# Optimization experiments

Hardware: AMD Instinct MI355X
Metric: run time of the kernel (lower is better)

Reference implementation:

```python
import jax, jax.numpy as jnp
import numpy as np

DIM = 1024
HEADS = 16
DIM_HEAD = 64
INNER = HEADS * DIM_HEAD
ALPHA = 128.0
SCALE = DIM_HEAD ** -0.5 / ALPHA
EPS = 1e-5
MAX_NEG = -jnp.finfo(jnp.float32).max


def layernorm(x, g):
    # torch.var(unbiased=False) layernorm with learned gain, no bias
    mean = jnp.mean(x, axis=-1, keepdims=True)
    var = jnp.mean(jnp.square(x - mean), axis=-1, keepdims=True)
    return (x - mean) * jax.lax.rsqrt(var + EPS) * g


def setup_inputs() -> dict:
    key = jax.random.key(0)
    ks = jax.random.split(key, 8)
    b, n = 8, 1024
    x = jax.random.normal(ks[0], (b, n, DIM), dtype=jnp.float32)
    mask = jax.random.bernoulli(ks[1], 0.9, (b, n))  # bool padding mask
    g_in = jnp.ones((DIM,), jnp.float32)
    Wq = jax.random.normal(ks[2], (INNER, DIM), jnp.float32) * (DIM ** -0.5)
    Wkv = jax.random.normal(ks[3], (2 * DIM_HEAD, DIM), jnp.float32) * (DIM ** -0.5)
    null_kv = jax.random.normal(ks[4], (2, DIM_HEAD), jnp.float32)
    Wo = jax.random.normal(ks[5], (DIM, INNER), jnp.float32) * (INNER ** -0.5)
    g_out = jnp.ones((DIM,), jnp.float32)
    return {"x": x, "mask": mask, "g_in": g_in, "Wq": Wq, "Wkv": Wkv,
            "null_kv": null_kv, "Wo": Wo, "g_out": g_out}


def reference(x, mask, g_in, Wq, Wkv, null_kv, Wo, g_out):
    b, n, _ = x.shape
    context = x                      # context captured BEFORE norm
    xn = layernorm(x, g_in)
    q = (xn @ Wq.T).reshape(b, n, HEADS, DIM_HEAD).transpose(0, 2, 1, 3)  # b h n d
    q = q * SCALE
    kv = context @ Wkv.T             # b n 2d (single shared KV head: MQA)
    k, v = jnp.split(kv, 2, axis=-1)
    nk = jnp.broadcast_to(null_kv[0], (b, 1, DIM_HEAD))
    nv = jnp.broadcast_to(null_kv[1], (b, 1, DIM_HEAD))
    k = jnp.concatenate([nk, k], axis=1)   # b (n+1) d
    v = jnp.concatenate([nv, v], axis=1)
    sim = jnp.einsum('bhid,bjd->bhij', q, k)  # b h n (n+1)
    # padding mask, True prepended for null token
    m = jnp.pad(mask, ((0, 0), (1, 0)), constant_values=True)
    sim = jnp.where(m[:, None, None, :], sim, MAX_NEG)
    # causal mask: triu with offset j-i+1 = 2 (null token always visible)
    i, j = n, n + 1
    causal = jnp.triu(jnp.ones((i, j), bool), j - i + 1)
    sim = jnp.where(causal, MAX_NEG, sim)
    # pb-relax: subtract detached max, rescale by alpha, softmax
    sim = sim - jax.lax.stop_gradient(jnp.max(sim, axis=-1, keepdims=True))
    attn = jax.nn.softmax(sim * ALPHA, axis=-1)
    out = jnp.einsum('bhij,bjd->bhid', attn, v)
    out = out.transpose(0, 2, 1, 3).reshape(b, n, INNER)
    out = out @ Wo.T
    return layernorm(out, g_out)
```

## Files before the change

kernel.cpp:

```cpp
#include <hip/hip_runtime.h>
#include <hip/hip_bf16.h>

#define B_     8
#define N_     1024
#define DIM_   1024
#define HEADS_ 16
#define DH_    64
#define INNER_ 1024
#define NKEY_  1025
#define NTILE_ 34
#define NW_    34
#define ROWS_  8192
#define EPS_   1e-5f
#define QK_SCALE_ 0.1803368801111f
#define TILE_ELEMS_ 4096

typedef unsigned short u16;
typedef unsigned char  u8;
typedef unsigned int   u32;
typedef __attribute__((ext_vector_type(8)))  short bf16x8;
typedef __attribute__((ext_vector_type(4)))  float f32x4;
typedef __attribute__((ext_vector_type(16))) float f32x16;

__device__ __forceinline__ float bf2f(u16 u) {
    unsigned int x = ((unsigned int)u) << 16;
    return __uint_as_float(x);
}
__device__ __forceinline__ u16 f2bf(float f) {
    unsigned int x = __float_as_uint(f);
    x += 0x7FFFu + ((x >> 16) & 1u);
    return (u16)(x >> 16);
}
__device__ __forceinline__ float max3f(float a, float b, float c) {
    return fmaxf(fmaxf(a, b), c);
}
__device__ __forceinline__ float exp2fast(float x) {
    float r;
    asm("v_exp_f32 %0, %1" : "=v"(r) : "v"(x));
    return r;
}

#define MFMA16(a, b, c) __builtin_amdgcn_mfma_f32_16x16x32_bf16((a), (b), (c), 0, 0, 0)
#define MFMA32(a, b, c) __builtin_amdgcn_mfma_f32_32x32x16_bf16((a), (b), (c), 0, 0, 0)

__device__ __forceinline__ void gload16(const void* g, void* l) {
    __builtin_amdgcn_global_load_lds(
        (const __attribute__((address_space(1))) unsigned int*)g,
        (__attribute__((address_space(3))) unsigned int*)l, 16, 0, 0);
}

__device__ __forceinline__ u32 cvtpk(float lo, float hi) {
    u32 r;
    asm("v_cvt_pk_bf16_f32 %0, %1, %2" : "=v"(r) : "v"(lo), "v"(hi));
    return r;
}
__device__ __forceinline__ void plswap(u32& a, u32& b) {
    asm volatile("v_permlane32_swap_b32 %0, %1" : "+v"(a), "+v"(b));
}

__global__ void detect_mask(const unsigned int* __restrict__ m, int* __restrict__ flag) {
    if (threadIdx.x == 0 && blockIdx.x == 0) {
        int f = 0;
        for (int i = 0; i < 64; ++i) {
            unsigned int w = m[i];
            if (w == 0x3F800000u) { f = 2; break; }
            if (w > 1u) f = 1;
        }
        *flag = f;
    }
}

__global__ void build_bits(const void* __restrict__ mraw, const int* __restrict__ flag,
                           u32* __restrict__ vbits) {
    int tid = blockIdx.x * blockDim.x + threadIdx.x;
    if (tid >= B_ * NW_) return;
    int b = tid / NW_, wq = tid - b * NW_;
    int f = *flag;
    u32 bits = 0;
    for (int i = 0; i < 32; ++i) {
        int jp = wq * 32 + i;
        bool vis;
        if (jp == 0) vis = true;
        else if (jp < NKEY_) {
            int idx = b * N_ + jp - 1;
            if (f == 0)      vis = ((const int*)mraw)[idx] != 0;
            else if (f == 1) vis = ((const u8*)mraw)[idx] != 0;
            else             vis = ((const float*)mraw)[idx] != 0.0f;
        } else vis = false;
        if (vis) bits |= (1u << i);
    }
    vbits[tid] = bits;
}

__global__ void cvt_w(const float* __restrict__ wq, const float* __restrict__ wkv,
                      const float* __restrict__ wo, u16* __restrict__ q16,
                      u16* __restrict__ kv16, u16* __restrict__ o16) {
    int i = blockIdx.x * blockDim.x + threadIdx.x;
    const int NQ = INNER_ * DIM_ / 4, NKV = 128 * DIM_ / 4, NO = DIM_ * INNER_ / 4;
    const float* src; u16* dst; int off;
    if (i < NQ)            { src = wq;  dst = q16;  off = i; }
    else if (i < NQ + NKV) { src = wkv; dst = kv16; off = i - NQ; }
    else if (i < NQ + NKV + NO) { src = wo; dst = o16; off = i - NQ - NKV; }
    else return;
    float4 v = ((const float4*)src)[off];
    ushort4 u; u.x = f2bf(v.x); u.y = f2bf(v.y); u.z = f2bf(v.z); u.w = f2bf(v.w);
    ((ushort4*)dst)[off] = u;
}

template<int MODE>
__global__ __launch_bounds__(256)
void ln_rows(const void* __restrict__ xv, const float* __restrict__ g,
             void* __restrict__ outv, u16* __restrict__ raw16) {
    int row = blockIdx.x;
    int t = threadIdx.x;
    float v0, v1, v2, v3;
    if constexpr (MODE == 0) {
        float4 v = ((const float4*)((const float*)xv + (size_t)row * DIM_))[t];
        v0 = v.x; v1 = v.y; v2 = v.z; v3 = v.w;
    } else {
        ushort4 u = ((const ushort4*)((const u16*)xv + (size_t)row * DIM_))[t];
        v0 = bf2f(u.x); v1 = bf2f(u.y); v2 = bf2f(u.z); v3 = bf2f(u.w);
    }
    float s  = v0 + v1 + v2 + v3;
    float ss = v0*v0 + v1*v1 + v2*v2 + v3*v3;
#pragma unroll
    for (int off = 32; off > 0; off >>= 1) {
        s  += __shfl_down(s,  off, 64);
        ss += __shfl_down(ss, off, 64);
    }
    __shared__ float red[10];
    int wid = t >> 6, lane = t & 63;
    if (lane == 0) { red[wid] = s; red[4 + wid] = ss; }
    __syncthreads();
    if (t == 0) {
        float S  = red[0] + red[1] + red[2] + red[3];
        float SS = red[4] + red[5] + red[6] + red[7];
        float mean = S * (1.0f / DIM_);
        float var  = SS * (1.0f / DIM_) - mean * mean;
        red[8] = mean;
        red[9] = rsqrtf(var + EPS_);
    }
    __syncthreads();
    float mean = red[8], rs = red[9];
    float4 gv = ((const float4*)g)[t];
    float o0 = (v0 - mean) * rs * gv.x;
    float o1 = (v1 - mean) * rs * gv.y;
    float o2 = (v2 - mean) * rs * gv.z;
    float o3 = (v3 - mean) * rs * gv.w;
    if constexpr (MODE == 0) {
        ushort4 u; u.x = f2bf(o0); u.y = f2bf(o1); u.z = f2bf(o2); u.w = f2bf(o3);
        ((ushort4*)((u16*)outv + (size_t)row * DIM_))[t] = u;
        ushort4 rw; rw.x = f2bf(v0); rw.y = f2bf(v1); rw.z = f2bf(v2); rw.w = f2bf(v3);
        ((ushort4*)(raw16 + (size_t)row * DIM_))[t] = rw;
    } else {
        float4 u; u.x = o0; u.y = o1; u.z = o2; u.w = o3;
        ((float4*)((float*)outv + (size_t)row * DIM_))[t] = u;
    }
}

__global__ __launch_bounds__(256)
void proj_fused(const u16* __restrict__ xn, const u16* __restrict__ xraw,
                const u16* __restrict__ wq, const u16* __restrict__ wkv,
                u16* __restrict__ qout, float* __restrict__ kvout) {
    __shared__ u16 As[128 * 32];
    __shared__ u16 Bs[128 * 32];
    const bool iskv = (blockIdx.x == 8);
    const u16* A  = iskv ? xraw : xn;
    const u16* Bt = iskv ? wkv : wq;
    const int  n0 = iskv ? 0 : blockIdx.x * 128;
    const float scale = iskv ? 1.0f : QK_SCALE_;
    const int t = threadIdx.x;
    const int w = t >> 6, l = t & 63;
    const int col = l & 15, rg = l >> 4;
    const int wm = (w >> 1) * 64, wn = (w & 1) * 64;
    const int m0 = blockIdx.y * 128;
    const int slr = l >> 2;
    const int slc = (l & 3) * 8;
    f32x4 acc[4][4];
#pragma unroll
    for (int i = 0; i < 4; ++i)
#pragma unroll
        for (int j = 0; j < 4; ++j) acc[i][j] = f32x4{0.f, 0.f, 0.f, 0.f};

    const u16* Abase = A  + (size_t)m0 * DIM_;
    const u16* Bbase = Bt + (size_t)n0 * DIM_;
    for (int k0 = 0; k0 < DIM_; k0 += 32) {
        __syncthreads();
#pragma unroll
        for (int p = 0; p < 2; ++p) {
            int rb = w * 2 + p;
            gload16(Abase + (size_t)(rb * 16 + slr) * DIM_ + k0 + slc, &As[rb * 512]);
            gload16(Bbase + (size_t)(rb * 16 + slr) * DIM_ + k0 + slc, &Bs[rb * 512]);
        }
        __syncthreads();
        bf16x8 af[4], bf4[4];
#pragma unroll
        for (int mi = 0; mi < 4; ++mi)
            af[mi] = *(const bf16x8*)&As[(wm + mi * 16 + col) * 32 + rg * 8];
#pragma unroll
        for (int ni = 0; ni < 4; ++ni)
            bf4[ni] = *(const bf16x8*)&Bs[(wn + ni * 16 + col) * 32 + rg * 8];
#pragma unroll
        for (int mi = 0; mi < 4; ++mi)
#pragma unroll
            for (int ni = 0; ni < 4; ++ni)
                acc[mi][ni] = MFMA16(af[mi], bf4[ni], acc[mi][ni]);
    }
#pragma unroll
    for (int mi = 0; mi < 4; ++mi)
#pragma unroll
        for (int ni = 0; ni < 4; ++ni)
#pragma unroll
            for (int r = 0; r < 4; ++r) {
                size_t row = (size_t)(m0 + wm + mi * 16 + rg * 4 + r);
                int c = n0 + wn + ni * 16 + col;
                float vv = acc[mi][ni][r] * scale;
                if (iskv) kvout[row * 128 + c] = vv;
                else      qout[row * INNER_ + c] = f2bf(vv);
            }
}

__global__ __launch_bounds__(256)
void gemm_o(const u16* __restrict__ A, const u16* __restrict__ Bt,
            u16* __restrict__ Cv) {
    __shared__ u16 As[128 * 32];
    __shared__ u16 Bs[128 * 32];
    const int t = threadIdx.x;
    const int w = t >> 6, l = t & 63;
    const int col = l & 15, rg = l >> 4;
    const int wm = (w >> 1) * 64, wn = (w & 1) * 64;
    const int m0 = blockIdx.y * 128, n0 = blockIdx.x * 128;
    const int slr = l >> 2;
    const int slc = (l & 3) * 8;
    f32x4 acc[4][4];
#pragma unroll
    for (int i = 0; i < 4; ++i)
#pragma unroll
        for (int j = 0; j < 4; ++j) acc[i][j] = f32x4{0.f, 0.f, 0.f, 0.f};
    const u16* Abase = A  + (size_t)m0 * INNER_;
    const u16* Bbase = Bt + (size_t)n0 * INNER_;
    for (int k0 = 0; k0 < INNER_; k0 += 32) {
        __syncthreads();
#pragma unroll
        for (int p = 0; p < 2; ++p) {
            int rb = w * 2 + p;
            gload16(Abase + (size_t)(rb * 16 + slr) * INNER_ + k0 + slc, &As[rb * 512]);
            gload16(Bbase + (size_t)(rb * 16 + slr) * INNER_ + k0 + slc, &Bs[rb * 512]);
        }
        __syncthreads();
        bf16x8 af[4], bf4[4];
#pragma unroll
        for (int mi = 0; mi < 4; ++mi)
            af[mi] = *(const bf16x8*)&As[(wm + mi * 16 + col) * 32 + rg * 8];
#pragma unroll
        for (int ni = 0; ni < 4; ++ni)
            bf4[ni] = *(const bf16x8*)&Bs[(wn + ni * 16 + col) * 32 + rg * 8];
#pragma unroll
        for (int mi = 0; mi < 4; ++mi)
#pragma unroll
            for (int ni = 0; ni < 4; ++ni)
                acc[mi][ni] = MFMA16(af[mi], bf4[ni], acc[mi][ni]);
    }
#pragma unroll
    for (int mi = 0; mi < 4; ++mi)
#pragma unroll
        for (int ni = 0; ni < 4; ++ni)
#pragma unroll
            for (int r = 0; r < 4; ++r) {
                size_t row = (size_t)(m0 + wm + mi * 16 + rg * 4 + r);
                int c = n0 + wn + ni * 16 + col;
                Cv[row * DIM_ + c] = f2bf(acc[mi][ni][r]);
            }
}

__global__ __launch_bounds__(256)
void build_kv(const float* __restrict__ kvf, const float* __restrict__ nullkv,
              u16* __restrict__ KVt) {
    const int kt = blockIdx.x, b = blockIdx.y;
    const int t = threadIdx.x;
    const int k0 = kt * 32;
    u16* base = KVt + ((size_t)b * NTILE_ + kt) * TILE_ELEMS_;
    {
        int j = t >> 3;
        int d0 = (t & 7) * 8;
        int jp = k0 + j;
        float v[8];
        if (jp == 0) {
#pragma unroll
            for (int i = 0; i < 8; ++i) v[i] = nullkv[d0 + i];
        } else if (jp <= N_) {
            const float* r = kvf + ((size_t)b * N_ + jp - 1) * 128 + d0;
            float4 a = ((const float4*)r)[0], c = ((const float4*)r)[1];
            v[0]=a.x; v[1]=a.y; v[2]=a.z; v[3]=a.w; v[4]=c.x; v[5]=c.y; v[6]=c.z; v[7]=c.w;
        } else {
#pragma unroll
            for (int i = 0; i < 8; ++i) v[i] = 0.f;
        }
        ushort4 u0, u1;
        u0.x=f2bf(v[0]); u0.y=f2bf(v[1]); u0.z=f2bf(v[2]); u0.w=f2bf(v[3]);
        u1.x=f2bf(v[4]); u1.y=f2bf(v[5]); u1.z=f2bf(v[6]); u1.w=f2bf(v[7]);
        *(ushort4*)(base + j * 64 + d0)     = u0;
        *(ushort4*)(base + j * 64 + d0 + 4) = u1;
    }
    {
        int d = t >> 2;
        int j0 = (t & 3) * 8;
        u16 o8[8];
#pragma unroll
        for (int i = 0; i < 8; ++i) {
            int jp = k0 + j0 + i;
            float val = 0.f;
            if (jp == 0) val = nullkv[64 + d];
            else if (jp <= N_) val = kvf[((size_t)b * N_ + jp - 1) * 128 + 64 + d];
            o8[i] = f2bf(val);
        }
        u16* dst = base + 2048 + d * 32 + j0;
        ushort4 u0, u1;
        u0.x=o8[0]; u0.y=o8[1]; u0.z=o8[2]; u0.w=o8[3];
        u1.x=o8[4]; u1.y=o8[5]; u1.z=o8[6]; u1.w=o8[7];
        *(ushort4*)dst = u0;
        *(ushort4*)(dst + 4) = u1;
    }
}

__global__ __launch_bounds__(256)
void attn_un(const u16* __restrict__ Q, const u16* __restrict__ KVt,
             const u32* __restrict__ vbits, u16* __restrict__ Out) {
    const int t = threadIdx.x;
    const int w = t >> 6, l = t & 63;
    const int lo = l & 31, hi = l >> 5;
    const int fid = blockIdx.x;
    const int b  = fid & 7;
    const int hg = (fid >> 3) & 3;
    const int qt = 31 - (fid >> 5);
    const int h = hg * 4 + w;
    const int i0 = qt * 32;
    const int nst = (qt + 3) >> 1;

    bf16x8 qf[4];
    {
        const u16* qp = Q + ((size_t)(b * N_ + i0 + lo)) * INNER_ + h * DH_ + hi * 8;
#pragma unroll
        for (int dt = 0; dt < 4; ++dt) qf[dt] = *(const bf16x8*)(qp + dt * 16);
    }
    f32x16 o0, o1;
#pragma unroll
    for (int i = 0; i < 16; ++i) { o0[i] = 0.f; o1[i] = 0.f; }
    float m = -3.0e38f, lsum = 0.f;

    const u16* tbase = KVt + (size_t)b * NTILE_ * TILE_ELEMS_;
    const u32* vbp = vbits + b * NW_;
    const int koff  = lo * 64 + hi * 8;
    const int voff0 = 2048 + lo * 32 + hi * 8;
    const int voff1 = 2048 + (lo + 32) * 32 + hi * 8;

    for (int st = 0; st < nst; ++st) {
        const int kt0 = st * 2, kt1 = st * 2 + 1;
        const u16* tb0 = tbase + (size_t)kt0 * TILE_ELEMS_;
        const u16* tb1 = tbase + (size_t)kt1 * TILE_ELEMS_;
        bf16x8 kf0[4], kf1[4];
        kf0[0] = *(const bf16x8*)(tb0 + koff);
        kf0[1] = *(const bf16x8*)(tb0 + koff + 16);
        kf0[2] = *(const bf16x8*)(tb0 + koff + 32);
        kf0[3] = *(const bf16x8*)(tb0 + koff + 48);
        kf1[0] = *(const bf16x8*)(tb1 + koff);
        kf1[1] = *(const bf16x8*)(tb1 + koff + 16);
        kf1[2] = *(const bf16x8*)(tb1 + koff + 32);
        kf1[3] = *(const bf16x8*)(tb1 + koff + 48);

        u32 vb0 = vbp[kt0], vb1 = vbp[kt1];
        union { u32 wd[4]; bf16x8 v; } bias0, bias1, ones;
        bias0.wd[0] = (hi == 0 && !((vb0 >> lo) & 1u)) ? 0xC6E0u : 0u;
        bias0.wd[1] = 0; bias0.wd[2] = 0; bias0.wd[3] = 0;
        bias1.wd[0] = (hi == 0 && !((vb1 >> lo) & 1u)) ? 0xC6E0u : 0u;
        bias1.wd[1] = 0; bias1.wd[2] = 0; bias1.wd[3] = 0;
        ones.wd[0] = (hi == 0) ? 0x3F80u : 0u;
        ones.wd[1] = 0; ones.wd[2] = 0; ones.wd[3] = 0;

        f32x16 s0, s1;
        __builtin_amdgcn_s_setprio(1);
#pragma unroll
        for (int i = 0; i < 16; ++i) { s0[i] = 0.f; s1[i] = 0.f; }
        s0 = MFMA32(kf0[0], qf[0], s0);
        s1 = MFMA32(kf1[0], qf[0], s1);
        s0 = MFMA32(kf0[1], qf[1], s0);
        s1 = MFMA32(kf1[1], qf[1], s1);
        s0 = MFMA32(kf0[2], qf[2], s0);
        s1 = MFMA32(kf1[2], qf[2], s1);
        s0 = MFMA32(kf0[3], qf[3], s0);
        s1 = MFMA32(kf1[3], qf[3], s1);
        s0 = MFMA32(bias0.v, ones.v, s0);
        s1 = MFMA32(bias1.v, ones.v, s1);
        __builtin_amdgcn_s_setprio(0);

        float t0 = max3f(s0[0],  s0[1],  s0[2]);
        float t1 = max3f(s0[3],  s0[4],  s0[5]);
        float t2 = max3f(s0[6],  s0[7],  s0[8]);
        float t3 = max3f(s0[9],  s0[10], s0[11]);
        float t4 = max3f(s0[12], s0[13], s0[14]);
        float u0 = max3f(s1[0],  s1[1],  s1[2]);
        float u1 = max3f(s1[3],  s1[4],  s1[5]);
        float u2 = max3f(s1[6],  s1[7],  s1[8]);
        float u3 = max3f(s1[9],  s1[10], s1[11]);
        float u4 = max3f(s1[12], s1[13], s1[14]);
        float mt = fmaxf(max3f(max3f(t0, t1, t2), max3f(t3, t4, s0[15]),
                               max3f(u0, u1, u2)),
                         max3f(u3, u4, s1[15]));
        mt = fmaxf(mt, __shfl_xor(mt, 32, 64));
        if (!__all(mt <= m + 8.0f)) {
            float mn = fmaxf(m, mt);
            float c = exp2fast(m - mn);
            lsum *= c;
#pragma unroll
            for (int i = 0; i < 16; ++i) { o0[i] *= c; o1[i] *= c; }
            m = mn;
        }
        float p0[16], p1[16];
#pragma unroll
        for (int r = 0; r < 16; ++r) p0[r] = exp2fast(s0[r] - m);
#pragma unroll
        for (int r = 0; r < 16; ++r) p1[r] = exp2fast(s1[r] - m);
        if (kt0 >= qt) {
            int lim0 = i0 + lo + 1 - kt0 * 32 - 4 * hi;
#pragma unroll
            for (int r = 0; r < 16; ++r)
                if (((r & 3) + 8 * (r >> 2)) > lim0) p0[r] = 0.f;
        }
        if (kt1 >= qt) {
            int lim1 = i0 + lo + 1 - kt1 * 32 - 4 * hi;
#pragma unroll
            for (int r = 0; r < 16; ++r)
                if (((r & 3) + 8 * (r >> 2)) > lim1) p1[r] = 0.f;
        }
        float ls = ((((p0[0]+p0[1])+(p0[2]+p0[3])) + ((p0[4]+p0[5])+(p0[6]+p0[7])))
                 +  (((p0[8]+p0[9])+(p0[10]+p0[11])) + ((p0[12]+p0[13])+(p0[14]+p0[15]))))
                 + ((((p1[0]+p1[1])+(p1[2]+p1[3])) + ((p1[4]+p1[5])+(p1[6]+p1[7])))
                 +  (((p1[8]+p1[9])+(p1[10]+p1[11])) + ((p1[12]+p1[13])+(p1[14]+p1[15]))));
        ls += __shfl_xor(ls, 32, 64);
        lsum += ls;

        u32 a0 = cvtpk(p0[0],  p0[1]),  a2 = cvtpk(p0[4],  p0[5]);  plswap(a0, a2);
        u32 a1 = cvtpk(p0[2],  p0[3]),  a3 = cvtpk(p0[6],  p0[7]);  plswap(a1, a3);
        u32 a4 = cvtpk(p0[8],  p0[9]),  a6 = cvtpk(p0[12], p0[13]); plswap(a4, a6);
        u32 a5 = cvtpk(p0[10], p0[11]), a7 = cvtpk(p0[14], p0[15]); plswap(a5, a7);
        u32 c0 = cvtpk(p1[0],  p1[1]),  c2 = cvtpk(p1[4],  p1[5]);  plswap(c0, c2);
        u32 c1 = cvtpk(p1[2],  p1[3]),  c3 = cvtpk(p1[6],  p1[7]);  plswap(c1, c3);
        u32 c4 = cvtpk(p1[8],  p1[9]),  c6 = cvtpk(p1[12], p1[13]); plswap(c4, c6);
        u32 c5 = cvtpk(p1[10], p1[11]), c7 = cvtpk(p1[14], p1[15]); plswap(c5, c7);
        union { u32 wd[4]; bf16x8 v; } f0, f1, g0, g1;
        f0.wd[0] = a0; f0.wd[1] = a1; f0.wd[2] = a2; f0.wd[3] = a3;
        f1.wd[0] = a4; f1.wd[1] = a5; f1.wd[2] = a6; f1.wd[3] = a7;
        g0.wd[0] = c0; g0.wd[1] = c1; g0.wd[2] = c2; g0.wd[3] = c3;
        g1.wd[0] = c4; g1.wd[1] = c5; g1.wd[2] = c6; g1.wd[3] = c7;

        bf16x8 vf0[4], vf1[4];
        vf0[0] = *(const bf16x8*)(tb0 + voff0);
        vf0[1] = *(const bf16x8*)(tb0 + voff0 + 16);
        vf0[2] = *(const bf16x8*)(tb0 + voff1);
        vf0[3] = *(const bf16x8*)(tb0 + voff1 + 16);
        vf1[0] = *(const bf16x8*)(tb1 + voff0);
        vf1[1] = *(const bf16x8*)(tb1 + voff0 + 16);
        vf1[2] = *(const bf16x8*)(tb1 + voff1);
        vf1[3] = *(const bf16x8*)(tb1 + voff1 + 16);
        __builtin_amdgcn_s_setprio(1);
        o0 = MFMA32(vf0[0], f0.v, o0);
        o1 = MFMA32(vf0[2], f0.v, o1);
        o0 = MFMA32(vf0[1], f1.v, o0);
        o1 = MFMA32(vf0[3], f1.v, o1);
        o0 = MFMA32(vf1[0], g0.v, o0);
        o1 = MFMA32(vf1[2], g0.v, o1);
        o0 = MFMA32(vf1[1], g1.v, o0);
        o1 = MFMA32(vf1[3], g1.v, o1);
        __builtin_amdgcn_s_setprio(0);
    }

    float inv = 1.0f / lsum;
    u16* ob = Out + ((size_t)(b * N_ + i0 + lo)) * INNER_ + h * DH_;
#pragma unroll
    for (int dd = 0; dd < 2; ++dd)
#pragma unroll
        for (int g = 0; g < 4; ++g) {
            int d0 = dd * 32 + 8 * g + 4 * hi;
            float e0 = (dd ? o1[4*g+0] : o0[4*g+0]) * inv;
            float e1 = (dd ? o1[4*g+1] : o0[4*g+1]) * inv;
            float e2 = (dd ? o1[4*g+2] : o0[4*g+2]) * inv;
            float e3 = (dd ? o1[4*g+3] : o0[4*g+3]) * inv;
            ushort4 u; u.x = f2bf(e0); u.y = f2bf(e1); u.z = f2bf(e2); u.w = f2bf(e3);
            *(ushort4*)(ob + d0) = u;
        }
}

extern "C" void kernel_launch(void* const* d_in, const int* in_sizes, int n_in,
                              void* d_out, int out_size, void* d_ws, size_t ws_size,
                              hipStream_t stream) {
    const float* x       = (const float*)d_in[0];
    const void*  maskraw = d_in[1];
    const float* g_in    = (const float*)d_in[2];
    const float* Wq      = (const float*)d_in[3];
    const float* Wkv     = (const float*)d_in[4];
    const float* nullkv  = (const float*)d_in[5];
    const float* Wo      = (const float*)d_in[6];
    const float* g_out   = (const float*)d_in[7];
    float* out = (float*)d_out;

    char* ws = (char*)d_ws;
    size_t off = 0;
    auto alloc = [&](size_t bytes) {
        void* p = ws + off;
        off += (bytes + 255) & ~(size_t)255;
        return p;
    };
    int* flag   = (int*)alloc(4);
    u32* vbits  = (u32*)alloc((size_t)B_ * NW_ * 4);
    u16* wq16   = (u16*)alloc((size_t)INNER_ * DIM_ * 2);
    u16* wkv16  = (u16*)alloc((size_t)128 * DIM_ * 2);
    u16* wo16   = (u16*)alloc((size_t)DIM_ * INNER_ * 2);
    u16* bufA   = (u16*)alloc((size_t)ROWS_ * DIM_ * 2);
    u16* xb     = (u16*)alloc((size_t)ROWS_ * DIM_ * 2);
    u16* bufC   = (u16*)alloc((size_t)ROWS_ * INNER_ * 2);
    float* kvf  = (float*)alloc((size_t)ROWS_ * 128 * 4);
    u16* KVt    = (u16*)alloc((size_t)B_ * NTILE_ * TILE_ELEMS_ * 2);

    detect_mask<<<1, 64, 0, stream>>>((const unsigned int*)maskraw, flag);
    build_bits<<<2, 256, 0, stream>>>(maskraw, flag, vbits);

    cvt_w<<<2176, 256, 0, stream>>>(Wq, Wkv, Wo, wq16, wkv16, wo16);

    ln_rows<0><<<ROWS_, 256, 0, stream>>>(x, g_in, bufA, xb);

    proj_fused<<<dim3(9, ROWS_ / 128), 256, 0, stream>>>(
        bufA, xb, wq16, wkv16, bufC, kvf);

    build_kv<<<dim3(NTILE_, B_), 256, 0, stream>>>(kvf, nullkv, KVt);

    attn_un<<<1024, 256, 0, stream>>>(bufC, KVt, vbits, bufA);

    gemm_o<<<dim3(DIM_ / 128, ROWS_ / 128), 256, 0, stream>>>(bufA, wo16, bufC);

    ln_rows<1><<<ROWS_, 256, 0, stream>>>(bufC, g_out, out, nullptr);
}
```

Before: 169.3 us.

## Double GEMM K-tile to 64 with XOR-swizzled LDS and MFMA priority

Both bf16 GEMM kernels (the fused Q/KV projection and the output projection) now stage 64-wide K slices per iteration instead of 32, so the number of loop iterations and block barriers is halved. LDS rows are XOR-swizzled on 16-byte chunks to avoid bank conflicts on the fragment reads. The MFMA section is wrapped in s_setprio to favour matrix issue. LDS use doubles to 32 KB per block, which may reduce occupancy, and there is still no double buffering.

```diff
diff --git a/kernel.cpp b/kernel.cpp
--- a/kernel.cpp
+++ b/kernel.cpp
@@ -158,12 +158,22 @@
     }
 }
 
+__device__ __forceinline__ void stage64(const u16* __restrict__ src, int K,
+                                        u16* __restrict__ lds, int w, int l) {
+#pragma unroll
+    for (int p = 0; p < 4; ++p) {
+        int row = p * 32 + w * 8 + (l >> 3);
+        int kc  = 8 * ((l & 7) ^ (row & 7));
+        gload16(src + (size_t)row * K + kc, &lds[(p * 32 + w * 8) * 64]);
+    }
+}
+
 __global__ __launch_bounds__(256)
 void proj_fused(const u16* __restrict__ xn, const u16* __restrict__ xraw,
                 const u16* __restrict__ wq, const u16* __restrict__ wkv,
                 u16* __restrict__ qout, float* __restrict__ kvout) {
-    __shared__ u16 As[128 * 32];
-    __shared__ u16 Bs[128 * 32];
+    __shared__ u16 As[128 * 64];
+    __shared__ u16 Bs[128 * 64];
     const bool iskv = (blockIdx.x == 8);
     const u16* A  = iskv ? xraw : xn;
     const u16* Bt = iskv ? wkv : wq;
@@ -174,8 +184,6 @@
     const int col = l & 15, rg = l >> 4;
     const int wm = (w >> 1) * 64, wn = (w & 1) * 64;
     const int m0 = blockIdx.y * 128;
-    const int slr = l >> 2;
-    const int slc = (l & 3) * 8;
     f32x4 acc[4][4];
 #pragma unroll
     for (int i = 0; i < 4; ++i)
@@ -184,27 +192,35 @@
 
     const u16* Abase = A  + (size_t)m0 * DIM_;
     const u16* Bbase = Bt + (size_t)n0 * DIM_;
-    for (int k0 = 0; k0 < DIM_; k0 += 32) {
+    for (int k0 = 0; k0 < DIM_; k0 += 64) {
         __syncthreads();
-#pragma unroll
-        for (int p = 0; p < 2; ++p) {
-            int rb = w * 2 + p;
-            gload16(Abase + (size_t)(rb * 16 + slr) * DIM_ + k0 + slc, &As[rb * 512]);
-            gload16(Bbase + (size_t)(rb * 16 + slr) * DIM_ + k0 + slc, &Bs[rb * 512]);
-        }
+        stage64(Abase + k0, DIM_, As, w, l);
+        stage64(Bbase + k0, DIM_, Bs, w, l);
         __syncthreads();
-        bf16x8 af[4], bf4[4];
+        bf16x8 af[4][2], bf4[4][2];
+#pragma unroll
+        for (int mi = 0; mi < 4; ++mi) {
+            int r = wm + mi * 16 + col;
+            int sw = 8 * (r & 7);
+            af[mi][0] = *(const bf16x8*)&As[r * 64 + ((rg * 8) ^ sw)];
+            af[mi][1] = *(const bf16x8*)&As[r * 64 + ((32 + rg * 8) ^ sw)];
+        }
+#pragma unroll
+        for (int ni = 0; ni < 4; ++ni) {
+            int r = wn + ni * 16 + col;
+            int sw = 8 * (r & 7);
+            bf4[ni][0] = *(const bf16x8*)&Bs[r * 64 + ((rg * 8) ^ sw)];
+            bf4[ni][1] = *(const bf16x8*)&Bs[r * 64 + ((32 + rg * 8) ^ sw)];
+        }
+        __builtin_amdgcn_s_setprio(1);
 #pragma unroll
         for (int mi = 0; mi < 4; ++mi)
-            af[mi] = *(const bf16x8*)&As[(wm + mi * 16 + col) * 32 + rg * 8];
-#pragma unroll
-        for (int ni = 0; ni < 4; ++ni)
-            bf4[ni] = *(const bf16x8*)&Bs[(wn + ni * 16 + col) * 32 + rg * 8];
-#pragma unroll
-        for (int mi = 0; mi < 4; ++mi)
-#pragma unroll
-            for (int ni = 0; ni < 4; ++ni)
-                acc[mi][ni] = MFMA16(af[mi], bf4[ni], acc[mi][ni]);
+#pragma unroll
+            for (int ni = 0; ni < 4; ++ni) {
+                acc[mi][ni] = MFMA16(af[mi][0], bf4[ni][0], acc[mi][ni]);
+                acc[mi][ni] = MFMA16(af[mi][1], bf4[ni][1], acc[mi][ni]);
+            }
+        __builtin_amdgcn_s_setprio(0);
     }
 #pragma unroll
     for (int mi = 0; mi < 4; ++mi)
@@ -223,15 +239,13 @@
 __global__ __launch_bounds__(256)
 void gemm_o(const u16* __restrict__ A, const u16* __restrict__ Bt,
             u16* __restrict__ Cv) {
-    __shared__ u16 As[128 * 32];
-    __shared__ u16 Bs[128 * 32];
+    __shared__ u16 As[128 * 64];
+    __shared__ u16 Bs[128 * 64];
     const int t = threadIdx.x;
     const int w = t >> 6, l = t & 63;
     const int col = l & 15, rg = l >> 4;
     const int wm = (w >> 1) * 64, wn = (w & 1) * 64;
     const int m0 = blockIdx.y * 128, n0 = blockIdx.x * 128;
-    const int slr = l >> 2;
-    const int slc = (l & 3) * 8;
     f32x4 acc[4][4];
 #pragma unroll
     for (int i = 0; i < 4; ++i)
@@ -239,27 +253,35 @@
         for (int j = 0; j < 4; ++j) acc[i][j] = f32x4{0.f, 0.f, 0.f, 0.f};
     const u16* Abase = A  + (size_t)m0 * INNER_;
     const u16* Bbase = Bt + (size_t)n0 * INNER_;
-    for (int k0 = 0; k0 < INNER_; k0 += 32) {
+    for (int k0 = 0; k0 < INNER_; k0 += 64) {
         __syncthreads();
-#pragma unroll
-        for (int p = 0; p < 2; ++p) {
-            int rb = w * 2 + p;
-            gload16(Abase + (size_t)(rb * 16 + slr) * INNER_ + k0 + slc, &As[rb * 512]);
-            gload16(Bbase + (size_t)(rb * 16 + slr) * INNER_ + k0 + slc, &Bs[rb * 512]);
-        }
+        stage64(Abase + k0, INNER_, As, w, l);
+        stage64(Bbase + k0, INNER_, Bs, w, l);
         __syncthreads();
-        bf16x8 af[4], bf4[4];
+        bf16x8 af[4][2], bf4[4][2];
+#pragma unroll
+        for (int mi = 0; mi < 4; ++mi) {
+            int r = wm + mi * 16 + col;
+            int sw = 8 * (r & 7);
+            af[mi][0] = *(const bf16x8*)&As[r * 64 + ((rg * 8) ^ sw)];
+            af[mi][1] = *(const bf16x8*)&As[r * 64 + ((32 + rg * 8) ^ sw)];
+        }
+#pragma unroll
+        for (int ni = 0; ni < 4; ++ni) {
+            int r = wn + ni * 16 + col;
+            int sw = 8 * (r & 7);
+            bf4[ni][0] = *(const bf16x8*)&Bs[r * 64 + ((rg * 8) ^ sw)];
+            bf4[ni][1] = *(const bf16x8*)&Bs[r * 64 + ((32 + rg * 8) ^ sw)];
+        }
+        __builtin_amdgcn_s_setprio(1);
 #pragma unroll
         for (int mi = 0; mi < 4; ++mi)
-            af[mi] = *(const bf16x8*)&As[(wm + mi * 16 + col) * 32 + rg * 8];
-#pragma unroll
-        for (int ni = 0; ni < 4; ++ni)
-            bf4[ni] = *(const bf16x8*)&Bs[(wn + ni * 16 + col) * 32 + rg * 8];
-#pragma unroll
-        for (int mi = 0; mi < 4; ++mi)
-#pragma unroll
-            for (int ni = 0; ni < 4; ++ni)
-                acc[mi][ni] = MFMA16(af[mi], bf4[ni], acc[mi][ni]);
+#pragma unroll
+            for (int ni = 0; ni < 4; ++ni) {
+                acc[mi][ni] = MFMA16(af[mi][0], bf4[ni][0], acc[mi][ni]);
+                acc[mi][ni] = MFMA16(af[mi][1], bf4[ni][1], acc[mi][ni]);
+            }
+        __builtin_amdgcn_s_setprio(0);
     }
 #pragma unroll
     for (int mi = 0; mi < 4; ++mi)
```

Result: slower. 173.4 us (+2.4%).
